# Performance work log

Hardware: AMD Instinct MI355X
Metric: run time of the kernel (lower is better)

Reference implementation:

```python
import jax, jax.numpy as jnp
import numpy as np

B, S, D = 2, 2048, 1024
H, DK = 16, 64            # n_heads, d_k = d_model // n_heads
EXP = 4                   # pattern-separation expand_factor
ED = DK * EXP             # expanded_dim = 256
TOPK = 32                 # top-k kept after ReLU expansion
ALPHA = 0.05
TNT = 1.0                 # trace_norm_target


def setup_inputs() -> dict:
    key = jax.random.key(0)
    ks = jax.random.split(key, 8)
    sc = 1.0 / np.sqrt(D)
    x = jax.random.normal(ks[0], (B, S, D), jnp.float32)
    W_q = jax.random.normal(ks[1], (D, D), jnp.float32) * sc
    W_k = jax.random.normal(ks[2], (D, D), jnp.float32) * sc
    W_v = jax.random.normal(ks[3], (D, D), jnp.float32) * sc
    W_o = jax.random.normal(ks[4], (D, D), jnp.float32) * sc
    # trace buffers (non-zero so the trace read path actually matters)
    traces = jax.random.normal(ks[5], (H, DK, DK), jnp.float32) * 0.02
    value_traces = jax.random.normal(ks[6], (H, ED, DK), jnp.float32) * 0.02
    # frozen random expansion projection (dentate gyrus), W / sqrt(d_k)
    W_expand = jax.random.normal(ks[7], (DK, ED), jnp.float32) / np.sqrt(DK)
    return dict(x=x, W_q=W_q, W_k=W_k, W_v=W_v, W_o=W_o,
                traces=traces, value_traces=value_traces, W_expand=W_expand)


def _eff_alpha(T):
    # alpha / (1 + ||T_h||_F / trace_norm_target), shape (1, H, 1, 1)
    norms = jnp.sqrt(jnp.sum(T * T, axis=(1, 2)))
    return (ALPHA / (1.0 + norms / TNT)).reshape(1, -1, 1, 1)


def _forward(x, W_q, W_k, W_v, W_o, traces, value_traces, W_expand):
    b, s, d = x.shape
    def proj(W):
        return jnp.einsum('bsd,de->bse', x, W).reshape(b, s, H, DK).transpose(0, 2, 1, 3)
    Q, K, V = proj(W_q), proj(W_k), proj(W_v)  # (B, H, S, DK)

    scores = jnp.einsum('bhqd,bhkd->bhqk', Q, K)
    # score trace bias: alpha_eff * (Q @ T @ K^T)
    QT = jnp.einsum('bhqd,hde->bhqe', Q, traces)
    trace_scores = jnp.einsum('bhqe,bhke->bhqk', QT, K)
    scores = (scores + _eff_alpha(traces) * trace_scores) / np.sqrt(DK)
    A = jax.nn.softmax(scores, axis=-1)
    out = jnp.einsum('bhqk,bhkd->bhqd', A, V)

    # value trace read with use_key_q shift: address with previous token's Q
    Q_addr = jnp.concatenate([jnp.zeros_like(Q[:, :, :1, :]), Q[:, :, :-1, :]], axis=2)
    # pattern separation: frozen random expansion + ReLU + top-k sparsify
    Q_exp = jax.nn.relu(jnp.einsum('bhsd,de->bhse', Q_addr, W_expand))  # (B,H,S,ED)
    kth = jax.lax.top_k(Q_exp, TOPK)[0][..., -1:]
    Q_sparse = jnp.where(Q_exp >= kth, Q_exp, 0.0)  # == scatter of top-k vals (ties at 0 contribute 0)
    stored = jnp.einsum('bhse,hed->bhsd', Q_sparse, value_traces)
    out = out + _eff_alpha(value_traces) * stored

    out = out.transpose(0, 2, 1, 3).reshape(b, s, d)
    return jnp.einsum('bsd,de->bse', out, W_o)


def reference(x, W_q, W_k, W_v, W_o, traces, value_traces, W_expand):
    return _forward(x, W_q, W_k, W_v, W_o, traces, value_traces, W_expand)
```

## Files before the change

kernel.cpp:

```cpp
#include <hip/hip_runtime.h>
#include <stdint.h>

#define Bn 2
#define Sn 2048
#define Dn 1024
#define Hn 16
#define DKn 64
#define EDn 256

typedef __attribute__((ext_vector_type(8))) short bvec8;
typedef __attribute__((ext_vector_type(4))) float fvec4;

#define MFMA(a, b, c) __builtin_amdgcn_mfma_f32_16x16x32_bf16(a, b, c, 0, 0, 0)

__device__ __forceinline__ float b2f(unsigned short u) {
  return __uint_as_float(((unsigned)u) << 16);
}
__device__ __forceinline__ unsigned short f2b(float x) {
  unsigned u = __float_as_uint(x);
  u += 0x7fffu + ((u >> 16) & 1u);
  return (unsigned short)(u >> 16);
}

__global__ __launch_bounds__(256) void k_alphas(
    const float* __restrict__ traces, const float* __restrict__ vtr,
    float* __restrict__ alphas) {
  int blk = blockIdx.x;
  const float* base;
  int n;
  if (blk < 16) { base = traces + blk * DKn * DKn; n = DKn * DKn; }
  else          { base = vtr + (blk - 16) * EDn * DKn; n = EDn * DKn; }
  float s = 0.f;
  for (int i = threadIdx.x; i < n; i += 256) { float v = base[i]; s += v * v; }
  __shared__ float red[256];
  red[threadIdx.x] = s;
  __syncthreads();
  for (int off = 128; off > 0; off >>= 1) {
    if (threadIdx.x < off) red[threadIdx.x] += red[threadIdx.x + off];
    __syncthreads();
  }
  if (threadIdx.x == 0) alphas[blk] = 0.05f / (1.f + sqrtf(red[0]));
}

__global__ __launch_bounds__(256) void k_trW(
    const float* __restrict__ w0, const float* __restrict__ w1,
    const float* __restrict__ w2, const float* __restrict__ w3,
    unsigned short* __restrict__ dst) {
  int z = blockIdx.z;
  const float* src = (z == 0) ? w0 : ((z == 1) ? w1 : ((z == 2) ? w2 : w3));
  unsigned short* d = dst + (size_t)z * Dn * Dn;
  __shared__ unsigned short Tl[64][72];
  int tid = threadIdx.x;
  int k0 = blockIdx.y * 64, n0 = blockIdx.x * 64;
#pragma unroll
  for (int i = 0; i < 4; ++i) {
    int q = tid + 256 * i;
    int kr = q >> 4, c4 = q & 15;
    float4 v = *(const float4*)&src[(size_t)(k0 + kr) * Dn + n0 + 4 * c4];
    ushort4 u;
    u.x = f2b(v.x); u.y = f2b(v.y); u.z = f2b(v.z); u.w = f2b(v.w);
    *(ushort4*)&Tl[kr][4 * c4] = u;
  }
  __syncthreads();
#pragma unroll
  for (int i = 0; i < 4; ++i) {
    int q = tid + 256 * i;
    int nr = q >> 4, c4 = q & 15;
    ushort4 u;
    u.x = Tl[4 * c4 + 0][nr]; u.y = Tl[4 * c4 + 1][nr];
    u.z = Tl[4 * c4 + 2][nr]; u.w = Tl[4 * c4 + 3][nr];
    *(ushort4*)&d[(size_t)(n0 + nr) * Dn + k0 + 4 * c4] = u;
  }
}

__global__ __launch_bounds__(256) void k_mkM(const float* __restrict__ tr,
                                             const float* __restrict__ alph,
                                             unsigned short* __restrict__ Mt) {
  int h = blockIdx.x;
  float a = alph[h] * 0.125f;
  const float* th = tr + (size_t)h * DKn * DKn;
  unsigned short* mh = Mt + (size_t)h * DKn * DKn;
  for (int i = threadIdx.x; i < DKn * DKn; i += 256) {
    int e = i >> 6, k = i & 63;
    float v = a * th[(size_t)k * DKn + e] + ((e == k) ? 0.125f : 0.f);
    mh[i] = f2b(v);
  }
}

__global__ __launch_bounds__(256) void k_trE(const float* __restrict__ Wexp,
                                             unsigned short* __restrict__ WexpT) {
  int e0 = blockIdx.x * 64;
  __shared__ unsigned short Tl[64][72];
  int tid = threadIdx.x;
#pragma unroll
  for (int i = 0; i < 4; ++i) {
    int q = tid + 256 * i;
    int dr = q >> 4, c4 = q & 15;
    float4 v = *(const float4*)&Wexp[(size_t)dr * EDn + e0 + 4 * c4];
    ushort4 u;
    u.x = f2b(v.x); u.y = f2b(v.y); u.z = f2b(v.z); u.w = f2b(v.w);
    *(ushort4*)&Tl[dr][4 * c4] = u;
  }
  __syncthreads();
#pragma unroll
  for (int i = 0; i < 4; ++i) {
    int q = tid + 256 * i;
    int er = q >> 4, c4 = q & 15;
    ushort4 u;
    u.x = Tl[4 * c4 + 0][er]; u.y = Tl[4 * c4 + 1][er];
    u.z = Tl[4 * c4 + 2][er]; u.w = Tl[4 * c4 + 3][er];
    *(ushort4*)&WexpT[(size_t)(e0 + er) * DKn + 4 * c4] = u;
  }
}

__global__ __launch_bounds__(256) void k_trVT(const float* __restrict__ vtr,
                                              unsigned short* __restrict__ VTt) {
  int e0 = blockIdx.x * 64;
  int h = blockIdx.y;
  const float* src = vtr + (size_t)h * EDn * DKn;
  unsigned short* dst = VTt + (size_t)h * DKn * EDn;
  __shared__ unsigned short Tl[64][72];
  int tid = threadIdx.x;
#pragma unroll
  for (int i = 0; i < 4; ++i) {
    int q = tid + 256 * i;
    int er = q >> 4, c4 = q & 15;
    float4 v = *(const float4*)&src[(size_t)(e0 + er) * DKn + 4 * c4];
    ushort4 u;
    u.x = f2b(v.x); u.y = f2b(v.y); u.z = f2b(v.z); u.w = f2b(v.w);
    *(ushort4*)&Tl[er][4 * c4] = u;
  }
  __syncthreads();
#pragma unroll
  for (int i = 0; i < 4; ++i) {
    int q = tid + 256 * i;
    int dr = q >> 4, c4 = q & 15;
    ushort4 u;
    u.x = Tl[4 * c4 + 0][dr]; u.y = Tl[4 * c4 + 1][dr];
    u.z = Tl[4 * c4 + 2][dr]; u.w = Tl[4 * c4 + 3][dr];
    *(ushort4*)&dst[(size_t)dr * EDn + e0 + 4 * c4] = u;
  }
}

__global__ __launch_bounds__(256) void k_xb(const float* __restrict__ x,
                                            unsigned short* __restrict__ xb) {
  size_t i = ((size_t)blockIdx.x * 256 + threadIdx.x) * 4;
  float4 v = *(const float4*)&x[i];
  ushort4 u;
  u.x = f2b(v.x); u.y = f2b(v.y); u.z = f2b(v.z); u.w = f2b(v.w);
  *(ushort4*)&xb[i] = u;
}

template <int MODE>
__global__ __launch_bounds__(256) void k_gemm(
    const unsigned short* __restrict__ Ab, const float* __restrict__ Af,
    const unsigned short* __restrict__ BtBase, unsigned short* __restrict__ Qb,
    unsigned short* __restrict__ Kb, unsigned short* __restrict__ Vb,
    float* __restrict__ Cout) {
  const int z = (MODE == 0) ? blockIdx.z : 0;
  const unsigned short* Bt = BtBase + (size_t)z * Dn * Dn;
  unsigned short* Cb =
      (MODE == 0) ? ((z == 0) ? Qb : ((z == 1) ? Kb : Vb)) : nullptr;
  __shared__ unsigned short As[128][40];
  __shared__ unsigned short Bs[128][40];
  const int tid = threadIdx.x;
  const int w = tid >> 6, lane = tid & 63, qd = lane >> 4, cc = lane & 15;
  const int m0 = blockIdx.y * 128, n0 = blockIdx.x * 128;
  const int mW = 64 * (w >> 1), nW = 64 * (w & 1);
  fvec4 acc[4][4];
#pragma unroll
  for (int i = 0; i < 4; ++i)
#pragma unroll
    for (int j = 0; j < 4; ++j) acc[i][j] = (fvec4){0.f, 0.f, 0.f, 0.f};

  for (int k0 = 0; k0 < Dn; k0 += 32) {
    if (MODE == 0) {
#pragma unroll
      for (int i = 0; i < 2; ++i) {
        int q = tid + 256 * i;
        int row = q >> 2, c8 = q & 3;
        *(uint4*)&As[row][8 * c8] =
            *(const uint4*)&Ab[(size_t)(m0 + row) * Dn + k0 + 8 * c8];
      }
    } else {
#pragma unroll
      for (int i = 0; i < 4; ++i) {
        int q = tid + 256 * i;
        int row = q >> 3, c4 = q & 7;
        float4 v = *(const float4*)&Af[(size_t)(m0 + row) * Dn + k0 + 4 * c4];
        ushort4 u;
        u.x = f2b(v.x); u.y = f2b(v.y); u.z = f2b(v.z); u.w = f2b(v.w);
        *(ushort4*)&As[row][4 * c4] = u;
      }
    }
#pragma unroll
    for (int i = 0; i < 2; ++i) {
      int q = tid + 256 * i;
      int row = q >> 2, c8 = q & 3;
      *(uint4*)&Bs[row][8 * c8] =
          *(const uint4*)&Bt[(size_t)(n0 + row) * Dn + k0 + 8 * c8];
    }
    __syncthreads();
    bvec8 af[4], bf[4];
#pragma unroll
    for (int i = 0; i < 4; ++i) {
      af[i] = *(const bvec8*)&As[mW + 16 * i + cc][8 * qd];
      bf[i] = *(const bvec8*)&Bs[nW + 16 * i + cc][8 * qd];
    }
#pragma unroll
    for (int i = 0; i < 4; ++i)
#pragma unroll
      for (int j = 0; j < 4; ++j) acc[i][j] = MFMA(af[i], bf[j], acc[i][j]);
    __syncthreads();
  }
#pragma unroll
  for (int i = 0; i < 4; ++i)
#pragma unroll
    for (int j = 0; j < 4; ++j)
#pragma unroll
      for (int r = 0; r < 4; ++r) {
        int row = m0 + mW + 16 * i + 4 * qd + r;
        int col = n0 + nW + 16 * j + cc;
        if (MODE == 0) {
          int b = row >> 11, s = row & 2047, h = col >> 6, dk = col & 63;
          Cb[(((size_t)(b * Hn + h)) * Sn + s) * DKn + dk] = f2b(acc[i][j][r]);
        } else {
          Cout[(size_t)row * Dn + col] = acc[i][j][r];
        }
      }
}

__global__ __launch_bounds__(256) void k_vtrans(
    const unsigned short* __restrict__ Vb, unsigned short* __restrict__ Vt) {
  int bh = blockIdx.x, st = blockIdx.y;
  __shared__ unsigned short Tl[64][72];
  int tid = threadIdx.x;
#pragma unroll
  for (int i = 0; i < 4; ++i) {
    int q = tid + 256 * i;
    int sr = q >> 4, c4 = q & 15;
    *(ushort4*)&Tl[sr][4 * c4] =
        *(const ushort4*)&Vb[((size_t)bh * Sn + st * 64 + sr) * DKn + 4 * c4];
  }
  __syncthreads();
#pragma unroll
  for (int i = 0; i < 4; ++i) {
    int q = tid + 256 * i;
    int dr = q >> 4, c4 = q & 15;
    ushort4 u;
    u.x = Tl[4 * c4 + 0][dr]; u.y = Tl[4 * c4 + 1][dr];
    u.z = Tl[4 * c4 + 2][dr]; u.w = Tl[4 * c4 + 3][dr];
    *(ushort4*)&Vt[((size_t)bh * DKn + dr) * Sn + st * 64 + 4 * c4] = u;
  }
}

__global__ __launch_bounds__(256, 2) void k_pattsep(
    const unsigned short* __restrict__ Qb,
    const unsigned short* __restrict__ WexpT,
    const unsigned short* __restrict__ VTt,
    const float* __restrict__ alphas, float* __restrict__ AT) {
  __shared__ uint4 Wl4[2048];
  __shared__ uint4 Vl4[2048];
  __shared__ uint4 Ps4[4][256];
  const int tile = blockIdx.x, bh = blockIdx.y;
  const int b = bh >> 4, h = bh & 15;
  const int tid = threadIdx.x;
  const int w = tid >> 6, lane = tid & 63, qd = lane >> 4, cc = lane & 15;
  const float avt = alphas[16 + h];

  const uint4* wsrc = (const uint4*)WexpT;
  const uint4* vsrc = (const uint4*)(VTt + (size_t)h * DKn * EDn);
  for (int i = tid; i < 2048; i += 256) {
    int e = i >> 3, c = i & 7;
    Wl4[e * 8 + (c ^ (e & 7))] = wsrc[i];
    int d = i >> 5, c2 = i & 31;
    Vl4[d * 32 + (c2 ^ (d & 7))] = vsrc[i];
  }
  __syncthreads();

  const unsigned short* Wls = (const unsigned short*)Wl4;
  const unsigned short* Vls = (const unsigned short*)Vl4;
  unsigned short* Pw = (unsigned short*)Ps4[w];

  for (int rg = 0; rg < 2; ++rg) {
    const int s0 = tile * 128 + w * 32 + rg * 16;
    bvec8 aq0 = {}, aq1 = {};
    const int srow = s0 + cc;
    if (srow > 0) {
      const unsigned short* qp = Qb + ((size_t)bh * Sn + srow - 1) * DKn;
      aq0 = *(const bvec8*)&qp[8 * qd];
      aq1 = *(const bvec8*)&qp[32 + 8 * qd];
    }
    fvec4 E[16];
#pragma unroll
    for (int j = 0; j < 16; ++j) {
      const int e = 16 * j + cc;
      const unsigned short* wr = Wls + e * 64;
      bvec8 b0 = *(const bvec8*)&wr[8 * (qd ^ (e & 7))];
      bvec8 b1 = *(const bvec8*)&wr[8 * ((4 + qd) ^ (e & 7))];
      fvec4 z = {0.f, 0.f, 0.f, 0.f};
      z = MFMA(aq0, b0, z);
      E[j] = MFMA(aq1, b1, z);
    }
#pragma unroll
    for (int j = 0; j < 16; ++j)
#pragma unroll
      for (int r = 0; r < 4; ++r) E[j][r] = fmaxf(E[j][r], 0.f);

    float thr[4];
#pragma unroll
    for (int r = 0; r < 4; ++r) {
      unsigned cur = 0u;
      bool done = false;
      for (int bit = 30; bit >= 0; --bit) {
        unsigned cand = cur | (1u << bit);
        float t = __uint_as_float(cand);
        int cnt = 0;
#pragma unroll
        for (int j = 0; j < 16; ++j) cnt += (E[j][r] >= t) ? 1 : 0;
        cnt += __shfl_xor(cnt, 1);
        cnt += __shfl_xor(cnt, 2);
        cnt += __shfl_xor(cnt, 4);
        cnt += __shfl_xor(cnt, 8);
        if (!done && cnt >= 32) {
          cur = cand;
          if (cnt == 32) done = true;
        }
        if (__all(done)) break;
      }
      thr[r] = __uint_as_float(cur);
    }

    fvec4 acc2[4];
#pragma unroll
    for (int j2 = 0; j2 < 4; ++j2) acc2[j2] = (fvec4){0.f, 0.f, 0.f, 0.f};

#pragma unroll
    for (int half = 0; half < 2; ++half) {
#pragma unroll
      for (int j = 0; j < 8; ++j) {
        const int jj = j + 8 * half;
#pragma unroll
        for (int r = 0; r < 4; ++r) {
          float v = E[jj][r];
          bool sel = (v >= thr[r]) && (v > 0.f);
          int row = 4 * qd + r;
          int s = 16 * j + cc;
          int ch = (s >> 3) ^ (row & 7);
          Pw[row * 128 + ch * 8 + (s & 7)] = sel ? f2b(v) : (unsigned short)0;
        }
      }
#pragma unroll
      for (int j2 = 0; j2 < 4; ++j2) {
        const int d = 16 * j2 + cc;
        const unsigned short* vr = Vls + d * 256;
#pragma unroll
        for (int c = 0; c < 4; ++c) {
          int cg = 4 * (c + 4 * half) + qd;
          bvec8 bv = *(const bvec8*)&vr[8 * (cg ^ (d & 7))];
          int ca = 4 * c + qd;
          bvec8 ap = *(const bvec8*)&Pw[cc * 128 + 8 * (ca ^ (cc & 7))];
          acc2[j2] = MFMA(ap, bv, acc2[j2]);
        }
      }
    }
#pragma unroll
    for (int j2 = 0; j2 < 4; ++j2)
#pragma unroll
      for (int r = 0; r < 4; ++r) {
        int row = s0 + 4 * qd + r;
        AT[((size_t)(b * Sn + row)) * Dn + h * DKn + 16 * j2 + cc] =
            avt * acc2[j2][r];
      }
  }
}

__global__ __launch_bounds__(256) void k_attn(
    const unsigned short* __restrict__ Qb, const unsigned short* __restrict__ Kb,
    const unsigned short* __restrict__ Vt, const unsigned short* __restrict__ Mt,
    float* __restrict__ AT) {
  __shared__ unsigned short Kd[64][72];
  __shared__ unsigned short Vl[64][72];
  __shared__ unsigned short Ps[4][16][72];
  const int bh = blockIdx.x, qt = blockIdx.y;
  const int b = bh >> 4, h = bh & 15;
  const int tid = threadIdx.x;
  const int w = tid >> 6, lane = tid & 63, qd = lane >> 4, cc = lane & 15;
  const float L2E = 1.4426950408889634f;
  const float NB = 23.083120654223414f;

  const unsigned short* qg = Qb + ((size_t)bh * Sn + qt * 64 + w * 16) * DKn;
  bvec8 a0 = *(const bvec8*)&qg[cc * DKn + 8 * qd];
  bvec8 a1 = *(const bvec8*)&qg[cc * DKn + 32 + 8 * qd];
  const unsigned short* mh = Mt + (size_t)h * DKn * DKn;
  unsigned short(*Qd)[72] = &Kd[16 * w];
#pragma unroll
  for (int j = 0; j < 4; ++j) {
    bvec8 b0 = *(const bvec8*)&mh[(size_t)(16 * j + cc) * DKn + 8 * qd];
    bvec8 b1 = *(const bvec8*)&mh[(size_t)(16 * j + cc) * DKn + 32 + 8 * qd];
    fvec4 z = {0.f, 0.f, 0.f, 0.f};
    z = MFMA(a0, b0, z);
    z = MFMA(a1, b1, z);
#pragma unroll
    for (int r = 0; r < 4; ++r) Qd[4 * qd + r][16 * j + cc] = f2b(z[r]);
  }
  bvec8 aq0 = *(const bvec8*)&Qd[cc][8 * qd];
  bvec8 aq1 = *(const bvec8*)&Qd[cc][32 + 8 * qd];

  float l_i[4] = {0.f, 0.f, 0.f, 0.f};
  fvec4 O[4];
#pragma unroll
  for (int j = 0; j < 4; ++j) O[j] = (fvec4){0.f, 0.f, 0.f, 0.f};

  for (int kt = 0; kt < Sn / 64; ++kt) {
    __syncthreads();
#pragma unroll
    for (int i = 0; i < 2; ++i) {
      int q = tid + 256 * i;
      int r = q >> 3, c8 = q & 7;
      *(uint4*)&Kd[r][8 * c8] =
          *(const uint4*)&Kb[((size_t)bh * Sn + kt * 64 + r) * DKn + 8 * c8];
      *(uint4*)&Vl[r][8 * c8] =
          *(const uint4*)&Vt[((size_t)bh * DKn + r) * Sn + kt * 64 + 8 * c8];
    }
    __syncthreads();
    fvec4 sc[4];
#pragma unroll
    for (int j = 0; j < 4; ++j) {
      bvec8 b0 = *(const bvec8*)&Kd[16 * j + cc][8 * qd];
      bvec8 b1 = *(const bvec8*)&Kd[16 * j + cc][32 + 8 * qd];
      fvec4 z = {0.f, 0.f, 0.f, 0.f};
      z = MFMA(aq0, b0, z);
      sc[j] = MFMA(aq1, b1, z);
    }
#pragma unroll
    for (int j = 0; j < 4; ++j)
#pragma unroll
      for (int r = 0; r < 4; ++r) {
        float p = exp2f(fmaf(sc[j][r], L2E, -NB));
        l_i[r] += p;
        Ps[w][4 * qd + r][16 * j + cc] = f2b(p);
      }
    bvec8 ap0 = *(const bvec8*)&Ps[w][cc][8 * qd];
    bvec8 ap1 = *(const bvec8*)&Ps[w][cc][32 + 8 * qd];
#pragma unroll
    for (int j = 0; j < 4; ++j) {
      bvec8 v0 = *(const bvec8*)&Vl[16 * j + cc][8 * qd];
      bvec8 v1 = *(const bvec8*)&Vl[16 * j + cc][32 + 8 * qd];
      O[j] = MFMA(ap0, v0, O[j]);
      O[j] = MFMA(ap1, v1, O[j]);
    }
  }
#pragma unroll
  for (int r = 0; r < 4; ++r) {
    l_i[r] += __shfl_xor(l_i[r], 1);
    l_i[r] += __shfl_xor(l_i[r], 2);
    l_i[r] += __shfl_xor(l_i[r], 4);
    l_i[r] += __shfl_xor(l_i[r], 8);
  }
  float inv[4];
#pragma unroll
  for (int r = 0; r < 4; ++r) inv[r] = 1.f / l_i[r];
#pragma unroll
  for (int j = 0; j < 4; ++j)
#pragma unroll
    for (int r = 0; r < 4; ++r) {
      int row = qt * 64 + w * 16 + 4 * qd + r;
      float* p = AT + ((size_t)(b * Sn + row)) * Dn + h * DKn + 16 * j + cc;
      *p += O[j][r] * inv[r];
    }
}

extern "C" void kernel_launch(void* const* d_in, const int* in_sizes, int n_in,
                              void* d_out, int out_size, void* d_ws,
                              size_t ws_size, hipStream_t stream) {
  const float* x = (const float*)d_in[0];
  const float* Wq = (const float*)d_in[1];
  const float* Wk = (const float*)d_in[2];
  const float* Wv = (const float*)d_in[3];
  const float* Wo = (const float*)d_in[4];
  const float* traces = (const float*)d_in[5];
  const float* vtr = (const float*)d_in[6];
  const float* Wexp = (const float*)d_in[7];

  const size_t NQ = (size_t)Bn * Hn * Sn * DKn;
  unsigned short* Qb = (unsigned short*)d_ws;
  unsigned short* Kb = Qb + NQ;
  unsigned short* Vb = Kb + NQ;
  unsigned short* Vt = Vb + NQ;
  unsigned short* Wt = Vt + NQ;
  unsigned short* Mt = Wt + NQ;
  unsigned short* WexpT = Mt + 65536;
  unsigned short* VTt = WexpT + 16384;
  float* alph = (float*)(VTt + 262144);
  float* AT = alph + 32;
  unsigned short* xb = (unsigned short*)AT;

  k_alphas<<<32, 256, 0, stream>>>(traces, vtr, alph);
  k_trW<<<dim3(16, 16, 4), 256, 0, stream>>>(Wq, Wk, Wv, Wo, Wt);
  k_mkM<<<16, 256, 0, stream>>>(traces, alph, Mt);
  k_trE<<<4, 256, 0, stream>>>(Wexp, WexpT);
  k_trVT<<<dim3(4, 16), 256, 0, stream>>>(vtr, VTt);
  k_xb<<<4096, 256, 0, stream>>>(x, xb);
  k_gemm<0><<<dim3(8, 32, 3), 256, 0, stream>>>(xb, nullptr, Wt, Qb, Kb, Vb,
                                                nullptr);
  k_vtrans<<<dim3(32, 32), 256, 0, stream>>>(Vb, Vt);
  k_pattsep<<<dim3(16, 32), 256, 0, stream>>>(Qb, WexpT, VTt, alph, AT);
  k_attn<<<dim3(32, 32), 256, 0, stream>>>(Qb, Kb, Vt, Mt, AT);
  k_gemm<1><<<dim3(8, 32, 1), 256, 0, stream>>>(
      nullptr, AT, Wt + 3 * (size_t)Dn * Dn, nullptr, nullptr, nullptr,
      (float*)d_out);
}
```

Before: 338.5 us.

## Use direct global-to-LDS loads with XOR swizzle and fuse V transpose into GEMM

Replaces register-staged global→LDS copies in the projection GEMM and attention kernels with global_load_lds 16-byte direct loads into unpadded, XOR-swizzled shared tiles. The V projection epilogue now writes the transposed (dk, s) layout directly, which removes the separate k_vtrans kernel and its extra pass over V. This aims to cut load instruction overhead, LDS bank conflicts and one launch plus round trip. The swizzle indexing must match the direct-load lane mapping exactly, and the transposed V stores are 4-element strided writes that may coalesce less well.

Result: faster. 324.2 us (-4.2%).

```diff
diff --git a/kernel.cpp b/kernel.cpp
--- a/kernel.cpp
+++ b/kernel.cpp
@@ -20,6 +20,11 @@
   unsigned u = __float_as_uint(x);
   u += 0x7fffu + ((u >> 16) & 1u);
   return (unsigned short)(u >> 16);
+}
+__device__ __forceinline__ void g2l(const unsigned short* g, unsigned short* l) {
+  __builtin_amdgcn_global_load_lds(
+      (const __attribute__((address_space(1))) void*)g,
+      (__attribute__((address_space(3))) void*)l, 16, 0, 0);
 }
 
 __global__ __launch_bounds__(256) void k_alphas(
@@ -155,18 +160,19 @@
 __global__ __launch_bounds__(256) void k_gemm(
     const unsigned short* __restrict__ Ab, const float* __restrict__ Af,
     const unsigned short* __restrict__ BtBase, unsigned short* __restrict__ Qb,
-    unsigned short* __restrict__ Kb, unsigned short* __restrict__ Vb,
+    unsigned short* __restrict__ Kb, unsigned short* __restrict__ VtOut,
     float* __restrict__ Cout) {
   const int z = (MODE == 0) ? blockIdx.z : 0;
   const unsigned short* Bt = BtBase + (size_t)z * Dn * Dn;
-  unsigned short* Cb =
-      (MODE == 0) ? ((z == 0) ? Qb : ((z == 1) ? Kb : Vb)) : nullptr;
-  __shared__ unsigned short As[128][40];
-  __shared__ unsigned short Bs[128][40];
+  __shared__ unsigned short As[128 * 32];
+  __shared__ unsigned short Bs[128 * 32];
   const int tid = threadIdx.x;
   const int w = tid >> 6, lane = tid & 63, qd = lane >> 4, cc = lane & 15;
   const int m0 = blockIdx.y * 128, n0 = blockIdx.x * 128;
   const int mW = 64 * (w >> 1), nW = 64 * (w & 1);
+  const int srow = lane >> 2;
+  const int schk = 8 * ((lane & 3) ^ (srow & 3));
+  const int r0 = 32 * w + srow, r1 = r0 + 16;
   fvec4 acc[4][4];
 #pragma unroll
   for (int i = 0; i < 4; ++i)
@@ -175,13 +181,8 @@
 
   for (int k0 = 0; k0 < Dn; k0 += 32) {
     if (MODE == 0) {
-#pragma unroll
-      for (int i = 0; i < 2; ++i) {
-        int q = tid + 256 * i;
-        int row = q >> 2, c8 = q & 3;
-        *(uint4*)&As[row][8 * c8] =
-            *(const uint4*)&Ab[(size_t)(m0 + row) * Dn + k0 + 8 * c8];
-      }
+      g2l(&Ab[(size_t)(m0 + r0) * Dn + k0 + schk], &As[1024 * w]);
+      g2l(&Ab[(size_t)(m0 + r1) * Dn + k0 + schk], &As[1024 * w + 512]);
     } else {
 #pragma unroll
       for (int i = 0; i < 4; ++i) {
@@ -190,22 +191,20 @@
         float4 v = *(const float4*)&Af[(size_t)(m0 + row) * Dn + k0 + 4 * c4];
         ushort4 u;
         u.x = f2b(v.x); u.y = f2b(v.y); u.z = f2b(v.z); u.w = f2b(v.w);
-        *(ushort4*)&As[row][4 * c4] = u;
-      }
-    }
-#pragma unroll
-    for (int i = 0; i < 2; ++i) {
-      int q = tid + 256 * i;
-      int row = q >> 2, c8 = q & 3;
-      *(uint4*)&Bs[row][8 * c8] =
-          *(const uint4*)&Bt[(size_t)(n0 + row) * Dn + k0 + 8 * c8];
-    }
+        *(ushort4*)&As[row * 32 + 8 * ((c4 >> 1) ^ (row & 3)) + 4 * (c4 & 1)] =
+            u;
+      }
+    }
+    g2l(&Bt[(size_t)(n0 + r0) * Dn + k0 + schk], &Bs[1024 * w]);
+    g2l(&Bt[(size_t)(n0 + r1) * Dn + k0 + schk], &Bs[1024 * w + 512]);
     __syncthreads();
     bvec8 af[4], bf[4];
 #pragma unroll
     for (int i = 0; i < 4; ++i) {
-      af[i] = *(const bvec8*)&As[mW + 16 * i + cc][8 * qd];
-      bf[i] = *(const bvec8*)&Bs[nW + 16 * i + cc][8 * qd];
+      int ra = mW + 16 * i + cc;
+      af[i] = *(const bvec8*)&As[ra * 32 + 8 * (qd ^ (ra & 3))];
+      int rb = nW + 16 * i + cc;
+      bf[i] = *(const bvec8*)&Bs[rb * 32 + 8 * (qd ^ (rb & 3))];
     }
 #pragma unroll
     for (int i = 0; i < 4; ++i)
@@ -216,42 +215,30 @@
 #pragma unroll
   for (int i = 0; i < 4; ++i)
 #pragma unroll
-    for (int j = 0; j < 4; ++j)
-#pragma unroll
-      for (int r = 0; r < 4; ++r) {
-        int row = m0 + mW + 16 * i + 4 * qd + r;
-        int col = n0 + nW + 16 * j + cc;
-        if (MODE == 0) {
-          int b = row >> 11, s = row & 2047, h = col >> 6, dk = col & 63;
-          Cb[(((size_t)(b * Hn + h)) * Sn + s) * DKn + dk] = f2b(acc[i][j][r]);
+    for (int j = 0; j < 4; ++j) {
+      int rowb = m0 + mW + 16 * i + 4 * qd;
+      int col = n0 + nW + 16 * j + cc;
+      if (MODE == 0) {
+        int b = rowb >> 11, s = rowb & 2047;
+        int h = col >> 6, dk = col & 63;
+        if (z == 2) {
+          ushort4 u;
+          u.x = f2b(acc[i][j][0]); u.y = f2b(acc[i][j][1]);
+          u.z = f2b(acc[i][j][2]); u.w = f2b(acc[i][j][3]);
+          *(ushort4*)&VtOut[(((size_t)(b * Hn + h)) * DKn + dk) * Sn + s] = u;
         } else {
-          Cout[(size_t)row * Dn + col] = acc[i][j][r];
+          unsigned short* Cb = (z == 0) ? Qb : Kb;
+#pragma unroll
+          for (int r = 0; r < 4; ++r)
+            Cb[(((size_t)(b * Hn + h)) * Sn + s + r) * DKn + dk] =
+                f2b(acc[i][j][r]);
         }
-      }
-}
-
-__global__ __launch_bounds__(256) void k_vtrans(
-    const unsigned short* __restrict__ Vb, unsigned short* __restrict__ Vt) {
-  int bh = blockIdx.x, st = blockIdx.y;
-  __shared__ unsigned short Tl[64][72];
-  int tid = threadIdx.x;
-#pragma unroll
-  for (int i = 0; i < 4; ++i) {
-    int q = tid + 256 * i;
-    int sr = q >> 4, c4 = q & 15;
-    *(ushort4*)&Tl[sr][4 * c4] =
-        *(const ushort4*)&Vb[((size_t)bh * Sn + st * 64 + sr) * DKn + 4 * c4];
-  }
-  __syncthreads();
-#pragma unroll
-  for (int i = 0; i < 4; ++i) {
-    int q = tid + 256 * i;
-    int dr = q >> 4, c4 = q & 15;
-    ushort4 u;
-    u.x = Tl[4 * c4 + 0][dr]; u.y = Tl[4 * c4 + 1][dr];
-    u.z = Tl[4 * c4 + 2][dr]; u.w = Tl[4 * c4 + 3][dr];
-    *(ushort4*)&Vt[((size_t)bh * DKn + dr) * Sn + st * 64 + 4 * c4] = u;
-  }
+      } else {
+#pragma unroll
+        for (int r = 0; r < 4; ++r)
+          Cout[(size_t)(rowb + r) * Dn + col] = acc[i][j][r];
+      }
+    }
 }
 
 __global__ __launch_bounds__(256, 2) void k_pattsep(
@@ -298,9 +285,9 @@
       const unsigned short* wr = Wls + e * 64;
       bvec8 b0 = *(const bvec8*)&wr[8 * (qd ^ (e & 7))];
       bvec8 b1 = *(const bvec8*)&wr[8 * ((4 + qd) ^ (e & 7))];
-      fvec4 z = {0.f, 0.f, 0.f, 0.f};
-      z = MFMA(aq0, b0, z);
-      E[j] = MFMA(aq1, b1, z);
+      fvec4 zv = {0.f, 0.f, 0.f, 0.f};
+      zv = MFMA(aq0, b0, zv);
+      E[j] = MFMA(aq1, b1, zv);
     }
 #pragma unroll
     for (int j = 0; j < 16; ++j)
@@ -379,8 +366,8 @@
     const unsigned short* __restrict__ Qb, const unsigned short* __restrict__ Kb,
     const unsigned short* __restrict__ Vt, const unsigned short* __restrict__ Mt,
     float* __restrict__ AT) {
-  __shared__ unsigned short Kd[64][72];
-  __shared__ unsigned short Vl[64][72];
+  __shared__ unsigned short Kd[64 * 64];
+  __shared__ unsigned short Vl[64 * 64];
   __shared__ unsigned short Ps[4][16][72];
   const int bh = blockIdx.x, qt = blockIdx.y;
   const int b = bh >> 4, h = bh & 15;
@@ -393,45 +380,52 @@
   bvec8 a0 = *(const bvec8*)&qg[cc * DKn + 8 * qd];
   bvec8 a1 = *(const bvec8*)&qg[cc * DKn + 32 + 8 * qd];
   const unsigned short* mh = Mt + (size_t)h * DKn * DKn;
-  unsigned short(*Qd)[72] = &Kd[16 * w];
 #pragma unroll
   for (int j = 0; j < 4; ++j) {
     bvec8 b0 = *(const bvec8*)&mh[(size_t)(16 * j + cc) * DKn + 8 * qd];
     bvec8 b1 = *(const bvec8*)&mh[(size_t)(16 * j + cc) * DKn + 32 + 8 * qd];
-    fvec4 z = {0.f, 0.f, 0.f, 0.f};
-    z = MFMA(a0, b0, z);
-    z = MFMA(a1, b1, z);
-#pragma unroll
-    for (int r = 0; r < 4; ++r) Qd[4 * qd + r][16 * j + cc] = f2b(z[r]);
-  }
-  bvec8 aq0 = *(const bvec8*)&Qd[cc][8 * qd];
-  bvec8 aq1 = *(const bvec8*)&Qd[cc][32 + 8 * qd];
+    fvec4 zz = {0.f, 0.f, 0.f, 0.f};
+    zz = MFMA(a0, b0, zz);
+    zz = MFMA(a1, b1, zz);
+#pragma unroll
+    for (int r = 0; r < 4; ++r) {
+      int qr = 4 * qd + r;
+      Kd[(16 * w + qr) * 64 + 8 * ((2 * j + (cc >> 3)) ^ (qr & 7)) + (cc & 7)] =
+          f2b(zz[r]);
+    }
+  }
+  bvec8 aq0 = *(const bvec8*)&Kd[(16 * w + cc) * 64 + 8 * (qd ^ (cc & 7))];
+  bvec8 aq1 =
+      *(const bvec8*)&Kd[(16 * w + cc) * 64 + 8 * ((qd + 4) ^ (cc & 7))];
 
   float l_i[4] = {0.f, 0.f, 0.f, 0.f};
   fvec4 O[4];
 #pragma unroll
   for (int j = 0; j < 4; ++j) O[j] = (fvec4){0.f, 0.f, 0.f, 0.f};
 
+  const int vrow = lane >> 3;
+  const int vchk = 8 * ((lane & 7) ^ (vrow & 7));
+  const unsigned short* kgb = Kb + (size_t)bh * Sn * DKn;
+  const unsigned short* vgb = Vt + (size_t)bh * DKn * Sn;
+
   for (int kt = 0; kt < Sn / 64; ++kt) {
     __syncthreads();
-#pragma unroll
-    for (int i = 0; i < 2; ++i) {
-      int q = tid + 256 * i;
-      int r = q >> 3, c8 = q & 7;
-      *(uint4*)&Kd[r][8 * c8] =
-          *(const uint4*)&Kb[((size_t)bh * Sn + kt * 64 + r) * DKn + 8 * c8];
-      *(uint4*)&Vl[r][8 * c8] =
-          *(const uint4*)&Vt[((size_t)bh * DKn + r) * Sn + kt * 64 + 8 * c8];
-    }
+    const unsigned short* kg = kgb + (size_t)kt * 64 * DKn;
+    g2l(&kg[(size_t)(16 * w + vrow) * 64 + vchk], &Kd[1024 * w]);
+    g2l(&kg[(size_t)(16 * w + 8 + vrow) * 64 + vchk], &Kd[1024 * w + 512]);
+    g2l(&vgb[(size_t)(16 * w + vrow) * Sn + kt * 64 + vchk], &Vl[1024 * w]);
+    g2l(&vgb[(size_t)(16 * w + 8 + vrow) * Sn + kt * 64 + vchk],
+        &Vl[1024 * w + 512]);
     __syncthreads();
     fvec4 sc[4];
 #pragma unroll
     for (int j = 0; j < 4; ++j) {
-      bvec8 b0 = *(const bvec8*)&Kd[16 * j + cc][8 * qd];
-      bvec8 b1 = *(const bvec8*)&Kd[16 * j + cc][32 + 8 * qd];
-      fvec4 z = {0.f, 0.f, 0.f, 0.f};
-      z = MFMA(aq0, b0, z);
-      sc[j] = MFMA(aq1, b1, z);
+      int rk = 16 * j + cc;
+      bvec8 b0 = *(const bvec8*)&Kd[rk * 64 + 8 * (qd ^ (cc & 7))];
+      bvec8 b1 = *(const bvec8*)&Kd[rk * 64 + 8 * ((qd + 4) ^ (cc & 7))];
+      fvec4 zz = {0.f, 0.f, 0.f, 0.f};
+      zz = MFMA(aq0, b0, zz);
+      sc[j] = MFMA(aq1, b1, zz);
     }
 #pragma unroll
     for (int j = 0; j < 4; ++j)
@@ -445,8 +439,9 @@
     bvec8 ap1 = *(const bvec8*)&Ps[w][cc][32 + 8 * qd];
 #pragma unroll
     for (int j = 0; j < 4; ++j) {
-      bvec8 v0 = *(const bvec8*)&Vl[16 * j + cc][8 * qd];
-      bvec8 v1 = *(const bvec8*)&Vl[16 * j + cc][32 + 8 * qd];
+      int rv = 16 * j + cc;
+      bvec8 v0 = *(const bvec8*)&Vl[rv * 64 + 8 * (qd ^ (cc & 7))];
+      bvec8 v1 = *(const bvec8*)&Vl[rv * 64 + 8 * ((qd + 4) ^ (cc & 7))];
       O[j] = MFMA(ap0, v0, O[j]);
       O[j] = MFMA(ap1, v1, O[j]);
     }
@@ -486,8 +481,7 @@
   const size_t NQ = (size_t)Bn * Hn * Sn * DKn;
   unsigned short* Qb = (unsigned short*)d_ws;
   unsigned short* Kb = Qb + NQ;
-  unsigned short* Vb = Kb + NQ;
-  unsigned short* Vt = Vb + NQ;
+  unsigned short* Vt = Kb + NQ;
   unsigned short* Wt = Vt + NQ;
   unsigned short* Mt = Wt + NQ;
   unsigned short* WexpT = Mt + 65536;
@@ -502,9 +496,8 @@
   k_trE<<<4, 256, 0, stream>>>(Wexp, WexpT);
   k_trVT<<<dim3(4, 16), 256, 0, stream>>>(vtr, VTt);
   k_xb<<<4096, 256, 0, stream>>>(x, xb);
-  k_gemm<0><<<dim3(8, 32, 3), 256, 0, stream>>>(xb, nullptr, Wt, Qb, Kb, Vb,
+  k_gemm<0><<<dim3(8, 32, 3), 256, 0, stream>>>(xb, nullptr, Wt, Qb, Kb, Vt,
                                                 nullptr);
-  k_vtrans<<<dim3(32, 32), 256, 0, stream>>>(Vb, Vt);
   k_pattsep<<<dim3(16, 32), 256, 0, stream>>>(Qb, WexpT, VTt, alph, AT);
   k_attn<<<dim3(32, 32), 256, 0, stream>>>(Qb, Kb, Vt, Mt, AT);
   k_gemm<1><<<dim3(8, 32, 1), 256, 0, stream>>>(
```
